# Performance work log

Measured on AMD Instinct MI355X. Metric: run time of the kernel, lower is better.

The kernel has to match this reference:

```python
import jax, jax.numpy as jnp
import numpy as np

B, T, I, H = 64, 256, 1024, 512


def _gru_layer(x, w_ih, w_hh, b_ih, b_hh):
    """PyTorch-semantics GRU layer, batch_first, h0=0.
    x: [B, T, In]; w_ih: [3H, In]; w_hh: [3H, H]; biases: [3H].
    Gate order (torch): r, z, n.
    """
    h_dim = w_hh.shape[1]
    # precompute input projections for all timesteps: [B, T, 3H]
    gx = jnp.einsum('bti,gi->btg', x, w_ih) + b_ih

    def step(h, gx_t):
        gh = h @ w_hh.T + b_hh                      # [B, 3H]
        xr, xz, xn = jnp.split(gx_t, 3, axis=-1)
        hr, hz, hn = jnp.split(gh, 3, axis=-1)
        r = jax.nn.sigmoid(xr + hr)
        z = jax.nn.sigmoid(xz + hz)
        n = jnp.tanh(xn + r * hn)
        h_new = (1.0 - z) * n + z * h
        return h_new, h_new

    h0 = jnp.zeros((x.shape[0], h_dim), x.dtype)
    _, out = jax.lax.scan(step, h0, jnp.swapaxes(gx, 0, 1))  # out: [T, B, H]
    return jnp.swapaxes(out, 0, 1)                            # [B, T, H]


def setup_inputs() -> dict:
    key = jax.random.key(0)
    ks = jax.random.split(key, 9)
    s1 = 1.0 / np.sqrt(H)   # torch GRU init: U(-1/sqrt(H), 1/sqrt(H)) of layer's hidden
    s2 = 1.0 / np.sqrt(I)
    u = lambda k, shp, s: jax.random.uniform(k, shp, jnp.float32, -s, s)
    return {
        'x': jax.random.normal(ks[0], (B, T, I), jnp.float32),
        'w_ih1': u(ks[1], (3 * H, I), s1),
        'w_hh1': u(ks[2], (3 * H, H), s1),
        'b_ih1': u(ks[3], (3 * H,), s1),
        'b_hh1': u(ks[4], (3 * H,), s1),
        'w_ih2': u(ks[5], (3 * I, H), s2),
        'w_hh2': u(ks[6], (3 * I, I), s2),
        'b_ih2': u(ks[7], (3 * I,), s2),
        'b_hh2': u(ks[8], (3 * I,), s2),
    }


def reference(x, w_ih1, w_hh1, b_ih1, b_hh1, w_ih2, w_hh2, b_ih2, b_hh2):
    h1 = _gru_layer(x, w_ih1, w_hh1, b_ih1, b_hh1)   # [B, T, H]
    h1 = jax.nn.relu(h1)
    out = _gru_layer(h1, w_ih2, w_hh2, b_ih2, b_hh2)  # [B, T, I]
    return out
```

## Files before the change

kernel.cpp:

```cpp
#include <hip/hip_runtime.h>

typedef _Float16 half_t;
typedef _Float16 half8  __attribute__((ext_vector_type(8)));
typedef float    f32x4  __attribute__((ext_vector_type(4)));
typedef int      i32x4  __attribute__((ext_vector_type(4)));

#define NB 64
#define NT 256
#define NI 1024
#define NH 512

__device__ __forceinline__ void gload16_cc(i32x4& v, const void* p) {
    asm volatile("global_load_dwordx4 %0, %1, off sc0 sc1"
                 : "=v"(v) : "v"(p) : "memory");
}
__device__ __forceinline__ void gstore16_cc(void* p, i32x4 v) {
    asm volatile("global_store_dwordx4 %0, %1, off sc0 sc1"
                 :: "v"(p), "v"(v) : "memory");
}

__device__ __forceinline__ void flag_barrier(unsigned* slots, int nslots,
                                             int my, unsigned gen, int tid) {
    if (tid < 64) {
        asm volatile("s_waitcnt vmcnt(0)" ::: "memory");
        if (tid == 0) {
            unsigned gv = gen;
            asm volatile("global_store_dword %0, %1, off sc0 sc1"
                         :: "v"(slots + my), "v"(gv) : "memory");
        }
        const unsigned* p = slots + (tid & (nslots - 1));
        int guard = 0;
        while (true) {
            unsigned v;
            asm volatile("global_load_dword %0, %1, off sc0 sc1"
                         : "=v"(v) : "v"(p) : "memory");
            asm volatile("s_waitcnt vmcnt(0)" ::: "memory");
            if (__all(v >= gen)) break;
            if (++guard > (1 << 24)) break;
        }
    }
    __syncthreads();
}

__global__ __launch_bounds__(256) void k_cvt(const float* __restrict__ s,
                                             half_t* __restrict__ d, int n4) {
    int i = blockIdx.x * 256 + threadIdx.x;
    if (i < n4) {
        float4 v = reinterpret_cast<const float4*>(s)[i];
        half_t h4[4] = {(half_t)v.x, (half_t)v.y, (half_t)v.z, (half_t)v.w};
        *reinterpret_cast<long*>(&d[i * 4]) = *reinterpret_cast<long*>(h4);
    }
}

template <int K, bool AF32>
__global__ __launch_bounds__(256) void k_gemm(const void* __restrict__ Av,
                                              const half_t* __restrict__ Bw,
                                              const float* __restrict__ bias,
                                              half_t* __restrict__ C, int N, int ldc) {
    constexpr int BK = 64;
    __shared__ half_t Al[2][128 * BK] __attribute__((aligned(16)));
    __shared__ half_t Bl[2][128 * BK] __attribute__((aligned(16)));

    const int tid = threadIdx.x, lane = tid & 63, wv = tid >> 6;
    const long m0 = (long)blockIdx.y * 128;
    const long n0 = (long)blockIdx.x * 128;
    const int wm = (wv >> 1) * 64, wn = (wv & 1) * 64;

    f32x4 acc[4][4];
#pragma unroll
    for (int nt = 0; nt < 4; ++nt) {
        float bv = bias[n0 + wn + nt * 16 + (lane & 15)];
#pragma unroll
        for (int mt = 0; mt < 4; ++mt) acc[mt][nt] = (f32x4){bv, bv, bv, bv};
    }

    auto stage = [&](int buf, int kt) {
#pragma unroll
        for (int j = 0; j < 4; ++j) {
            int c = tid + 256 * j;
            int row = c >> 3, cin = c & 7;
            int dst = row * BK + ((cin ^ (row & 7)) << 3);
            if constexpr (AF32) {
                const float* Af = (const float*)Av;
                const float* src = Af + (m0 + row) * K + kt * BK + cin * 8;
                float4 f0 = *reinterpret_cast<const float4*>(src);
                float4 f1 = *reinterpret_cast<const float4*>(src + 4);
                half8 h;
                h[0] = (half_t)f0.x; h[1] = (half_t)f0.y; h[2] = (half_t)f0.z; h[3] = (half_t)f0.w;
                h[4] = (half_t)f1.x; h[5] = (half_t)f1.y; h[6] = (half_t)f1.z; h[7] = (half_t)f1.w;
                *reinterpret_cast<half8*>(&Al[buf][dst]) = h;
            } else {
                const half_t* Ah = (const half_t*)Av;
                *reinterpret_cast<int4*>(&Al[buf][dst]) =
                    *reinterpret_cast<const int4*>(Ah + (m0 + row) * K + kt * BK + cin * 8);
            }
            *reinterpret_cast<int4*>(&Bl[buf][dst]) =
                *reinterpret_cast<const int4*>(Bw + (n0 + row) * K + kt * BK + cin * 8);
        }
    };

    stage(0, 0);
    __syncthreads();
    constexpr int NK = K / BK;
    int buf = 0;
    for (int kt = 0; kt < NK; ++kt) {
        if (kt + 1 < NK) stage(buf ^ 1, kt + 1);
        half8 af[4][2], bf[4][2];
#pragma unroll
        for (int mt = 0; mt < 4; ++mt)
#pragma unroll
            for (int ks = 0; ks < 2; ++ks) {
                int lr = wm + mt * 16 + (lane & 15);
                int off = lr * BK + ((ks * 32 + 8 * (lane >> 4)) ^ ((lr & 7) << 3));
                af[mt][ks] = *reinterpret_cast<const half8*>(&Al[buf][off]);
            }
#pragma unroll
        for (int nt = 0; nt < 4; ++nt)
#pragma unroll
            for (int ks = 0; ks < 2; ++ks) {
                int lr = wn + nt * 16 + (lane & 15);
                int off = lr * BK + ((ks * 32 + 8 * (lane >> 4)) ^ ((lr & 7) << 3));
                bf[nt][ks] = *reinterpret_cast<const half8*>(&Bl[buf][off]);
            }
#pragma unroll
        for (int mt = 0; mt < 4; ++mt)
#pragma unroll
            for (int nt = 0; nt < 4; ++nt)
#pragma unroll
                for (int ks = 0; ks < 2; ++ks)
                    acc[mt][nt] = __builtin_amdgcn_mfma_f32_16x16x32_f16(
                        af[mt][ks], bf[nt][ks], acc[mt][nt], 0, 0, 0);
        __syncthreads();
        buf ^= 1;
    }
#pragma unroll
    for (int mt = 0; mt < 4; ++mt)
#pragma unroll
        for (int nt = 0; nt < 4; ++nt)
#pragma unroll
            for (int i = 0; i < 4; ++i) {
                long row = m0 + wm + mt * 16 + 4 * (lane >> 4) + i;
                long col = n0 + wn + nt * 16 + (lane & 15);
                C[row * (long)ldc + col] = (half_t)acc[mt][nt][i];
            }
}

__global__ __launch_bounds__(256, 1) void k_phase1(const half_t* __restrict__ whh,
                                                   const float* __restrict__ bhh,
                                                   const half_t* __restrict__ gx,
                                                   half_t* __restrict__ hrelu,
                                                   half_t* __restrict__ hf16,
                                                   unsigned* __restrict__ slots) {
    __shared__ half_t wl[48 * NH] __attribute__((aligned(16)));
    __shared__ half_t hl[16 * NH] __attribute__((aligned(16)));
    __shared__ float xch[3][8][16];
    __shared__ half_t hst[8][16] __attribute__((aligned(16)));

    const int tid = threadIdx.x, lane = tid & 63, wv = tid >> 6;
    const int g = blockIdx.x & 7, memb = blockIdx.x >> 3;
    const int e0 = memb * 16;
    unsigned* gslots = slots + g * 64;

#pragma unroll
    for (int j = 0; j < 12; ++j) {
        int c = tid + 256 * j;
        int lr = c >> 6, cin = c & 63;
        int grow = (lr >> 4) * NH + e0 + (lr & 15);
        int dst = lr * NH + ((cin ^ (lr & 7)) << 3);
        *reinterpret_cast<int4*>(&wl[dst]) =
            *reinterpret_cast<const int4*>(whh + (long)grow * NH + cin * 8);
    }
#pragma unroll
    for (int j = 0; j < 2; ++j) {
        int c = tid + 256 * j;
        int lr = 8 + (c >> 6), cin = c & 63;
        int4 z; z.x = z.y = z.z = z.w = 0;
        *reinterpret_cast<int4*>(&hl[lr * NH + cin * 8]) = z;
    }
    if (tid < 16) {
        i32x4 z = (i32x4){0, 0, 0, 0};
        int bb = tid >> 1, seg = tid & 1;
        gstore16_cc(hf16 + (g * 8 + bb) * NH + e0 + seg * 8, z);
    }
    float hp = 0.f, hrp = 0.f;
    __syncthreads();
    flag_barrier(gslots, 32, memb, 1, tid);

    const float bgate = (wv < 3) ? bhh[wv * NH + e0 + (lane & 15)] : 0.f;
    const int b = tid >> 4, e = tid & 15;
    const long rb0 = (long)(g * 8 + b) * NT;

    float xr = 0.f, xz = 0.f, xn = 0.f, nxr = 0.f, nxz = 0.f, nxn = 0.f;
    if (tid < 128) {
        long gb = rb0 * 1536 + e0 + e;
        xr = (float)gx[gb]; xz = (float)gx[gb + NH]; xn = (float)gx[gb + 2 * NH];
    }

    for (int t = 0; t < NT; ++t) {
        if (tid < 128 && t > 0)
            hrelu[(rb0 + t - 1) * NH + e0 + e] = (half_t)hrp;

        const half_t* hsrc = hf16 + (t & 1) * (NB * NH);
        i32x4 sv[2];
#pragma unroll
        for (int j = 0; j < 2; ++j) {
            int c = tid + 256 * j;
            int lr = c >> 6, cin = c & 63;
            gload16_cc(sv[j], hsrc + (g * 8 + lr) * NH + cin * 8);
        }
        asm volatile("s_waitcnt vmcnt(0)" ::: "memory");
#pragma unroll
        for (int j = 0; j < 2; ++j) {
            int c = tid + 256 * j;
            int lr = c >> 6, cin = c & 63;
            *reinterpret_cast<i32x4*>(&hl[lr * NH + ((cin ^ (lr & 7)) << 3)]) = sv[j];
        }
        __syncthreads();

        if (tid < 128 && t + 1 < NT) {
            long gb = (rb0 + t + 1) * 1536 + e0 + e;
            nxr = (float)gx[gb]; nxz = (float)gx[gb + NH]; nxn = (float)gx[gb + 2 * NH];
        }

        if (wv < 3) {
            f32x4 a0 = (f32x4){bgate, bgate, bgate, bgate};
            f32x4 a1 = (f32x4){0.f, 0.f, 0.f, 0.f};
#pragma unroll
            for (int ks = 0; ks < 16; ks += 2) {
                int ar = lane & 15;
                int br = wv * 16 + (lane & 15);
                int ao0 = ar * NH + ((ks * 32 + 8 * (lane >> 4)) ^ ((ar & 7) << 3));
                int bo0 = br * NH + ((ks * 32 + 8 * (lane >> 4)) ^ ((br & 7) << 3));
                int ao1 = ar * NH + (((ks + 1) * 32 + 8 * (lane >> 4)) ^ ((ar & 7) << 3));
                int bo1 = br * NH + (((ks + 1) * 32 + 8 * (lane >> 4)) ^ ((br & 7) << 3));
                a0 = __builtin_amdgcn_mfma_f32_16x16x32_f16(
                    *reinterpret_cast<const half8*>(&hl[ao0]),
                    *reinterpret_cast<const half8*>(&wl[bo0]), a0, 0, 0, 0);
                a1 = __builtin_amdgcn_mfma_f32_16x16x32_f16(
                    *reinterpret_cast<const half8*>(&hl[ao1]),
                    *reinterpret_cast<const half8*>(&wl[bo1]), a1, 0, 0, 0);
            }
            f32x4 acc = a0 + a1;
            if (lane < 32) {
#pragma unroll
                for (int i = 0; i < 4; ++i)
                    xch[wv][4 * (lane >> 4) + i][lane & 15] = acc[i];
            }
        }
        __syncthreads();

        if (tid < 128) {
            float r = 1.f / (1.f + __expf(-(xr + xch[0][b][e])));
            float z = 1.f / (1.f + __expf(-(xz + xch[1][b][e])));
            float n = tanhf(xn + r * xch[2][b][e]);
            float hn = (1.f - z) * n + z * hp;
            hp = hn;
            hrp = fmaxf(hn, 0.f);
            hst[b][e] = (half_t)hn;
        }
        __syncthreads();

        if (t + 1 < NT) {
            if (tid < 16) {
                int bb = tid >> 1, seg = tid & 1;
                i32x4 v = *reinterpret_cast<const i32x4*>(&hst[bb][seg * 8]);
                gstore16_cc(hf16 + ((t + 1) & 1) * (NB * NH) + (g * 8 + bb) * NH + e0 + seg * 8, v);
            }
            flag_barrier(gslots, 32, memb, t + 2, tid);
        }
        xr = nxr; xz = nxz; xn = nxn;
    }
    if (tid < 128)
        hrelu[(rb0 + NT - 1) * NH + e0 + e] = (half_t)hrp;
}

__global__ __launch_bounds__(256, 1) void k_phase2(const half_t* __restrict__ whh,
                                                   const float* __restrict__ bhh,
                                                   const half_t* __restrict__ gx,
                                                   float* __restrict__ out,
                                                   half_t* __restrict__ hf16,
                                                   unsigned* __restrict__ slots) {
    __shared__ half_t wl[48 * NI] __attribute__((aligned(16)));
    __shared__ half_t hl[16 * NI] __attribute__((aligned(16)));
    __shared__ float xch2[3][16][16];
    __shared__ half_t hst[16][16] __attribute__((aligned(16)));

    const int tid = threadIdx.x, lane = tid & 63, wv = tid >> 6;
    const int xcd = blockIdx.x & 7;
    const int g = xcd >> 1;
    const int memb = ((blockIdx.x >> 3) << 1) | (xcd & 1);
    const int e0 = memb * 16;
    unsigned* gslots = slots + g * 64;

#pragma unroll
    for (int j = 0; j < 24; ++j) {
        int c = tid + 256 * j;
        int lr = c >> 7, cin = c & 127;
        int grow = (lr >> 4) * NI + e0 + (lr & 15);
        int dst = lr * NI + ((cin ^ (lr & 7)) << 3);
        *reinterpret_cast<int4*>(&wl[dst]) =
            *reinterpret_cast<const int4*>(whh + (long)grow * NI + cin * 8);
    }
    if (tid < 32) {
        i32x4 z = (i32x4){0, 0, 0, 0};
        int bb = tid >> 1, seg = tid & 1;
        gstore16_cc(hf16 + (g * 16 + bb) * NI + e0 + seg * 8, z);
    }
    float hp = 0.f;
    __syncthreads();
    flag_barrier(gslots, 64, memb, 1, tid);

    const float bgate = (wv < 3) ? bhh[wv * NI + e0 + (lane & 15)] : 0.f;
    const int b = tid >> 4, e = tid & 15;
    const long rb0 = (long)(g * 16 + b) * NT;

    float xr, xz, xn, nxr = 0.f, nxz = 0.f, nxn = 0.f;
    {
        long gb = rb0 * 3072 + e0 + e;
        xr = (float)gx[gb]; xz = (float)gx[gb + NI]; xn = (float)gx[gb + 2 * NI];
    }

    for (int t = 0; t < NT; ++t) {
        if (t > 0)
            out[(rb0 + t - 1) * NI + e0 + e] = hp;

        const half_t* hsrc = hf16 + (t & 1) * (NB * NI);
        i32x4 sv[8];
#pragma unroll
        for (int j = 0; j < 8; ++j) {
            int c = tid + 256 * j;
            int lr = c >> 7, cin = c & 127;
            gload16_cc(sv[j], hsrc + (g * 16 + lr) * NI + cin * 8);
        }
        asm volatile("s_waitcnt vmcnt(0)" ::: "memory");
#pragma unroll
        for (int j = 0; j < 8; ++j) {
            int c = tid + 256 * j;
            int lr = c >> 7, cin = c & 127;
            *reinterpret_cast<i32x4*>(&hl[lr * NI + ((cin ^ (lr & 7)) << 3)]) = sv[j];
        }
        __syncthreads();

        if (t + 1 < NT) {
            long gb = (rb0 + t + 1) * 3072 + e0 + e;
            nxr = (float)gx[gb]; nxz = (float)gx[gb + NI]; nxn = (float)gx[gb + 2 * NI];
        }

        if (wv < 3) {
            f32x4 a0 = (f32x4){bgate, bgate, bgate, bgate};
            f32x4 a1 = (f32x4){0.f, 0.f, 0.f, 0.f};
#pragma unroll
            for (int ks = 0; ks < 32; ks += 2) {
                int ar = lane & 15;
                int br = wv * 16 + (lane & 15);
                int ao0 = ar * NI + ((ks * 32 + 8 * (lane >> 4)) ^ ((ar & 7) << 3));
                int bo0 = br * NI + ((ks * 32 + 8 * (lane >> 4)) ^ ((br & 7) << 3));
                int ao1 = ar * NI + (((ks + 1) * 32 + 8 * (lane >> 4)) ^ ((ar & 7) << 3));
                int bo1 = br * NI + (((ks + 1) * 32 + 8 * (lane >> 4)) ^ ((br & 7) << 3));
                a0 = __builtin_amdgcn_mfma_f32_16x16x32_f16(
                    *reinterpret_cast<const half8*>(&hl[ao0]),
                    *reinterpret_cast<const half8*>(&wl[bo0]), a0, 0, 0, 0);
                a1 = __builtin_amdgcn_mfma_f32_16x16x32_f16(
                    *reinterpret_cast<const half8*>(&hl[ao1]),
                    *reinterpret_cast<const half8*>(&wl[bo1]), a1, 0, 0, 0);
            }
            f32x4 acc = a0 + a1;
#pragma unroll
            for (int i = 0; i < 4; ++i)
                xch2[wv][4 * (lane >> 4) + i][lane & 15] = acc[i];
        }
        __syncthreads();

        {
            float r = 1.f / (1.f + __expf(-(xr + xch2[0][b][e])));
            float z = 1.f / (1.f + __expf(-(xz + xch2[1][b][e])));
            float n = tanhf(xn + r * xch2[2][b][e]);
            float hn = (1.f - z) * n + z * hp;
            hp = hn;
            hst[b][e] = (half_t)hn;
        }
        __syncthreads();

        if (t + 1 < NT) {
            if (tid < 32) {
                int bb = tid >> 1, seg = tid & 1;
                i32x4 v = *reinterpret_cast<const i32x4*>(&hst[bb][seg * 8]);
                gstore16_cc(hf16 + ((t + 1) & 1) * (NB * NI) + (g * 16 + bb) * NI + e0 + seg * 8, v);
            }
            flag_barrier(gslots, 64, memb, t + 2, tid);
        }
        xr = nxr; xz = nxz; xn = nxn;
    }
    out[(rb0 + NT - 1) * NI + e0 + e] = hp;
}

extern "C" void kernel_launch(void* const* d_in, const int* in_sizes, int n_in,
                              void* d_out, int out_size, void* d_ws, size_t ws_size,
                              hipStream_t stream) {
    const float* x     = (const float*)d_in[0];
    const float* w_ih1 = (const float*)d_in[1];
    const float* w_hh1 = (const float*)d_in[2];
    const float* b_ih1 = (const float*)d_in[3];
    const float* b_hh1 = (const float*)d_in[4];
    const float* w_ih2 = (const float*)d_in[5];
    const float* w_hh2 = (const float*)d_in[6];
    const float* b_ih2 = (const float*)d_in[7];
    const float* b_hh2 = (const float*)d_in[8];

    char* ws = (char*)d_ws;
    unsigned* slots1 = (unsigned*)ws;
    unsigned* slots2 = (unsigned*)(ws + 2048);
    half_t* h1f16  = (half_t*)(ws + 4096);
    half_t* h2f16  = (half_t*)(ws + 135168);
    half_t* wih1h  = (half_t*)(ws + 1048576);
    half_t* whh1h  = (half_t*)(ws + 4194304);
    half_t* wih2h  = (half_t*)(ws + 5767168);
    half_t* whh2h  = (half_t*)(ws + 8912896);
    half_t* hrelu  = (half_t*)(ws + 16777216);
    half_t* gxU    = (half_t*)(ws + 50331648);
    float*  out    = (float*)d_out;

    hipMemsetAsync(ws, 0, 4096, stream);

    k_cvt<<<1536, 256, 0, stream>>>(w_ih1, wih1h, 393216);
    k_cvt<<<768,  256, 0, stream>>>(w_hh1, whh1h, 196608);
    k_cvt<<<1536, 256, 0, stream>>>(w_ih2, wih2h, 393216);
    k_cvt<<<3072, 256, 0, stream>>>(w_hh2, whh2h, 786432);

    k_gemm<1024, true><<<dim3(12, 128), 256, 0, stream>>>(x, wih1h, b_ih1, gxU, 1536, 1536);
    k_phase1<<<256, 256, 0, stream>>>(whh1h, b_hh1, gxU, hrelu, h1f16, slots1);
    k_gemm<512, false><<<dim3(24, 128), 256, 0, stream>>>(hrelu, wih2h, b_ih2, gxU, 3072, 3072);
    k_phase2<<<256, 256, 0, stream>>>(whh2h, b_hh2, gxU, out, h2f16, slots2);
}
```

Before: 2.533 ms.

## Fuse both GRU layers into one persistent kernel with wavefront pipelining

Replaces the separate layer-1 recurrence, layer-2 input GEMM and layer-2 recurrence kernels with one persistent kernel. Layer 1 runs on 64 blocks, and one wave per block computes the layer-2 input projection (with ReLU) one step behind. Layer 2 runs on 128 blocks split into two batch halves and follows layer 1 through flag waits, so the two recurrences overlap in time instead of running one after the other. It also adds s_sleep to the spin barrier. The cost is more cross-block synchronisation, a single wave carrying the extra GEMM work, and fewer blocks per recurrence group.

Result: slower. 3.281 ms (+29.5%).

```diff
diff --git a/kernel.cpp b/kernel.cpp
--- a/kernel.cpp
+++ b/kernel.cpp
@@ -9,6 +9,7 @@
 #define NT 256
 #define NI 1024
 #define NH 512
+#define MFMA16 __builtin_amdgcn_mfma_f32_16x16x32_f16
 
 __device__ __forceinline__ void gload16_cc(i32x4& v, const void* p) {
     asm volatile("global_load_dwordx4 %0, %1, off sc0 sc1"
@@ -17,6 +18,12 @@
 __device__ __forceinline__ void gstore16_cc(void* p, i32x4 v) {
     asm volatile("global_store_dwordx4 %0, %1, off sc0 sc1"
                  :: "v"(p), "v"(v) : "memory");
+}
+__device__ __forceinline__ unsigned gloadu16_cc(const void* p) {
+    unsigned v;
+    asm volatile("global_load_ushort %0, %1, off sc0 sc1"
+                 : "=v"(v) : "v"(p) : "memory");
+    return v;
 }
 
 __device__ __forceinline__ void flag_barrier(unsigned* slots, int nslots,
@@ -36,7 +43,8 @@
                          : "=v"(v) : "v"(p) : "memory");
             asm volatile("s_waitcnt vmcnt(0)" ::: "memory");
             if (__all(v >= gen)) break;
-            if (++guard > (1 << 24)) break;
+            __builtin_amdgcn_s_sleep(1);
+            if (++guard > (1 << 22)) break;
         }
     }
     __syncthreads();
@@ -52,8 +60,8 @@
     }
 }
 
-template <int K, bool AF32>
-__global__ __launch_bounds__(256) void k_gemm(const void* __restrict__ Av,
+template <int K>
+__global__ __launch_bounds__(256) void k_gemm(const float* __restrict__ Af,
                                               const half_t* __restrict__ Bw,
                                               const float* __restrict__ bias,
                                               half_t* __restrict__ C, int N, int ldc) {
@@ -80,20 +88,13 @@
             int c = tid + 256 * j;
             int row = c >> 3, cin = c & 7;
             int dst = row * BK + ((cin ^ (row & 7)) << 3);
-            if constexpr (AF32) {
-                const float* Af = (const float*)Av;
-                const float* src = Af + (m0 + row) * K + kt * BK + cin * 8;
-                float4 f0 = *reinterpret_cast<const float4*>(src);
-                float4 f1 = *reinterpret_cast<const float4*>(src + 4);
-                half8 h;
-                h[0] = (half_t)f0.x; h[1] = (half_t)f0.y; h[2] = (half_t)f0.z; h[3] = (half_t)f0.w;
-                h[4] = (half_t)f1.x; h[5] = (half_t)f1.y; h[6] = (half_t)f1.z; h[7] = (half_t)f1.w;
-                *reinterpret_cast<half8*>(&Al[buf][dst]) = h;
-            } else {
-                const half_t* Ah = (const half_t*)Av;
-                *reinterpret_cast<int4*>(&Al[buf][dst]) =
-                    *reinterpret_cast<const int4*>(Ah + (m0 + row) * K + kt * BK + cin * 8);
-            }
+            const float* src = Af + (m0 + row) * K + kt * BK + cin * 8;
+            float4 f0 = *reinterpret_cast<const float4*>(src);
+            float4 f1 = *reinterpret_cast<const float4*>(src + 4);
+            half8 h;
+            h[0] = (half_t)f0.x; h[1] = (half_t)f0.y; h[2] = (half_t)f0.z; h[3] = (half_t)f0.w;
+            h[4] = (half_t)f1.x; h[5] = (half_t)f1.y; h[6] = (half_t)f1.z; h[7] = (half_t)f1.w;
+            *reinterpret_cast<half8*>(&Al[buf][dst]) = h;
             *reinterpret_cast<int4*>(&Bl[buf][dst]) =
                 *reinterpret_cast<const int4*>(Bw + (n0 + row) * K + kt * BK + cin * 8);
         }
@@ -128,8 +129,7 @@
             for (int nt = 0; nt < 4; ++nt)
 #pragma unroll
                 for (int ks = 0; ks < 2; ++ks)
-                    acc[mt][nt] = __builtin_amdgcn_mfma_f32_16x16x32_f16(
-                        af[mt][ks], bf[nt][ks], acc[mt][nt], 0, 0, 0);
+                    acc[mt][nt] = MFMA16(af[mt][ks], bf[nt][ks], acc[mt][nt], 0, 0, 0);
         __syncthreads();
         buf ^= 1;
     }
@@ -145,253 +145,371 @@
             }
 }
 
-__global__ __launch_bounds__(256, 1) void k_phase1(const half_t* __restrict__ whh,
-                                                   const float* __restrict__ bhh,
-                                                   const half_t* __restrict__ gx,
-                                                   half_t* __restrict__ hrelu,
-                                                   half_t* __restrict__ hf16,
-                                                   unsigned* __restrict__ slots) {
-    __shared__ half_t wl[48 * NH] __attribute__((aligned(16)));
-    __shared__ half_t hl[16 * NH] __attribute__((aligned(16)));
-    __shared__ float xch[3][8][16];
-    __shared__ half_t hst[8][16] __attribute__((aligned(16)));
-
+__global__ __launch_bounds__(256, 1) void k_fused(
+    const half_t* __restrict__ whh1, const float* __restrict__ bhh1,
+    const half_t* __restrict__ wih2, const float* __restrict__ bih2,
+    const half_t* __restrict__ whh2, const float* __restrict__ bhh2,
+    half_t* gxU, float* __restrict__ out,
+    half_t* h1buf, half_t* h2buf,
+    unsigned* slots1, unsigned* slots2) {
+
+    __shared__ __attribute__((aligned(16))) char arena[160768];
     const int tid = threadIdx.x, lane = tid & 63, wv = tid >> 6;
-    const int g = blockIdx.x & 7, memb = blockIdx.x >> 3;
-    const int e0 = memb * 16;
-    unsigned* gslots = slots + g * 64;
-
-#pragma unroll
-    for (int j = 0; j < 12; ++j) {
-        int c = tid + 256 * j;
-        int lr = c >> 6, cin = c & 63;
-        int grow = (lr >> 4) * NH + e0 + (lr & 15);
-        int dst = lr * NH + ((cin ^ (lr & 7)) << 3);
-        *reinterpret_cast<int4*>(&wl[dst]) =
-            *reinterpret_cast<const int4*>(whh + (long)grow * NH + cin * 8);
+    const int bid = blockIdx.x;
+
+    if (bid < 64) {
+        half_t* wl   = (half_t*)arena;
+        half_t* wl2  = (half_t*)(arena + 32768);
+        half_t* hl   = (half_t*)(arena + 81920);
+        float*  xch  = (float* )(arena + 147456);
+        half_t* gxst = (half_t*)(arena + 153600);
+        half_t* hst  = (half_t*)(arena + 159744);
+        const int memb = bid, e0 = memb * 8;
+
+#pragma unroll
+        for (int j = 0; j < 8; ++j) {
+            int c = tid + 256 * j, lr = c >> 6, cin = c & 63;
+            i32x4 v = (i32x4){0, 0, 0, 0};
+            if (lr < 24)
+                v = *(const i32x4*)(whh1 + (long)((lr >> 3) * NH + e0 + (lr & 7)) * NH + cin * 8);
+            *(i32x4*)&wl[lr * NH + ((cin ^ (lr & 7)) << 3)] = v;
+        }
+#pragma unroll
+        for (int j = 0; j < 12; ++j) {
+            int c = tid + 256 * j, lr = c >> 6, cin = c & 63;
+            *(i32x4*)&wl2[lr * NH + ((cin ^ (lr & 7)) << 3)] =
+                *(const i32x4*)(wih2 + (long)(memb * 48 + lr) * NH + cin * 8);
+        }
+        if (tid < 64) {
+            i32x4 z = (i32x4){0, 0, 0, 0};
+            gstore16_cc(h1buf + tid * NH + e0, z);
+        }
+        __syncthreads();
+        flag_barrier(slots1, 64, memb, 1, tid);
+
+        const int e = tid & 7, b0 = tid >> 3, b1 = b0 + 32;
+        const float bh_r = bhh1[e0 + e], bh_z = bhh1[NH + e0 + e], bh_n = bhh1[2 * NH + e0 + e];
+        float bi2[3] = {0.f, 0.f, 0.f};
+        if (wv == 3) {
+#pragma unroll
+            for (int nt = 0; nt < 3; ++nt)
+                bi2[nt] = bih2[memb * 48 + nt * 16 + (lane & 15)];
+        }
+        float hp0 = 0.f, hp1 = 0.f;
+        const int cin = tid & 63, r0 = tid >> 6;
+
+        auto load_h = [&](int buf) {
+            i32x4 sv[16];
+            const half_t* hsrc = h1buf + buf * (NB * NH);
+#pragma unroll
+            for (int j = 0; j < 16; ++j)
+                gload16_cc(sv[j], hsrc + (r0 + 4 * j) * NH + cin * 8);
+            asm volatile("s_waitcnt vmcnt(0)" ::: "memory");
+            __builtin_amdgcn_sched_barrier(0);
+#pragma unroll
+            for (int j = 0; j < 16; ++j) {
+                int lr = r0 + 4 * j;
+                *(i32x4*)&hl[lr * NH + ((cin ^ (lr & 7)) << 3)] = sv[j];
+            }
+        };
+
+        auto wave3_gx2 = [&]() {
+            f32x4 g2[4][3];
+#pragma unroll
+            for (int mt = 0; mt < 4; ++mt)
+#pragma unroll
+                for (int nt = 0; nt < 3; ++nt) g2[mt][nt] = (f32x4){0.f, 0.f, 0.f, 0.f};
+#pragma unroll
+            for (int ks = 0; ks < 16; ++ks) {
+                int ko = ks * 32 + 8 * (lane >> 4);
+                half8 a[4];
+#pragma unroll
+                for (int mt = 0; mt < 4; ++mt) {
+                    int ar = mt * 16 + (lane & 15);
+                    a[mt] = *(const half8*)&hl[ar * NH + (ko ^ ((ar & 7) << 3))];
+#pragma unroll
+                    for (int jj = 0; jj < 8; ++jj)
+                        a[mt][jj] = a[mt][jj] > (half_t)0.f ? a[mt][jj] : (half_t)0.f;
+                }
+#pragma unroll
+                for (int nt = 0; nt < 3; ++nt) {
+                    int br = nt * 16 + (lane & 15);
+                    half8 bf = *(const half8*)&wl2[br * NH + (ko ^ ((br & 7) << 3))];
+#pragma unroll
+                    for (int mt = 0; mt < 4; ++mt)
+                        g2[mt][nt] = MFMA16(a[mt], bf, g2[mt][nt], 0, 0, 0);
+                }
+            }
+            int col = lane & 15, brow4 = 4 * (lane >> 4);
+#pragma unroll
+            for (int mt = 0; mt < 4; ++mt)
+#pragma unroll
+                for (int nt = 0; nt < 3; ++nt)
+#pragma unroll
+                    for (int i = 0; i < 4; ++i)
+                        gxst[(mt * 16 + brow4 + i) * 48 + nt * 16 + col] =
+                            (half_t)(g2[mt][nt][i] + bi2[nt]);
+        };
+
+        auto gx2_store = [&](int trow) {
+#pragma unroll
+            for (int rr = 0; rr < 6; ++rr) {
+                int c = tid + 64 * rr;
+                int bb = c / 6, kk = c - bb * 6;
+                gstore16_cc(gxU + ((long)bb * NT + trow) * 3072 + memb * 48 + kk * 8,
+                            *(i32x4*)&gxst[bb * 48 + kk * 8]);
+            }
+        };
+
+        for (int t = 0; t < NT; ++t) {
+            long g0 = ((long)b0 * NT + t) * 3072 + e0 + e;
+            long g1 = ((long)b1 * NT + t) * 3072 + e0 + e;
+            float xr0 = (float)gxU[g0], xz0 = (float)gxU[g0 + NH], xn0 = (float)gxU[g0 + 2 * NH];
+            float xr1 = (float)gxU[g1], xz1 = (float)gxU[g1 + NH], xn1 = (float)gxU[g1 + 2 * NH];
+            load_h(t & 1);
+            __syncthreads();
+
+            if (wv < 2) {
+#pragma unroll
+                for (int mt2 = 0; mt2 < 2; ++mt2) {
+                    const int mt = wv * 2 + mt2;
+                    f32x4 a0 = (f32x4){0, 0, 0, 0}, a1 = (f32x4){0, 0, 0, 0};
+#pragma unroll
+                    for (int ks = 0; ks < 16; ks += 2) {
+                        int ar = mt * 16 + (lane & 15);
+                        int br = lane & 15;
+                        int ko0 = ks * 32 + 8 * (lane >> 4), ko1 = ko0 + 32;
+                        a0 = MFMA16(*(const half8*)&hl[ar * NH + (ko0 ^ ((ar & 7) << 3))],
+                                    *(const half8*)&wl[br * NH + (ko0 ^ ((br & 7) << 3))], a0, 0, 0, 0);
+                        a1 = MFMA16(*(const half8*)&hl[ar * NH + (ko1 ^ ((ar & 7) << 3))],
+                                    *(const half8*)&wl[br * NH + (ko1 ^ ((br & 7) << 3))], a1, 0, 0, 0);
+                    }
+                    f32x4 acc = a0 + a1;
+                    int col = lane & 15, brow = mt * 16 + 4 * (lane >> 4);
+#pragma unroll
+                    for (int i = 0; i < 4; ++i) {
+                        if (col < 8) xch[(brow + i) * 8 + col] = acc[i];
+                        else         xch[512 + (brow + i) * 8 + (col - 8)] = acc[i];
+                    }
+                }
+            } else if (wv == 2) {
+#pragma unroll
+                for (int mt = 0; mt < 4; ++mt) {
+                    f32x4 a0 = (f32x4){0, 0, 0, 0}, a1 = (f32x4){0, 0, 0, 0};
+#pragma unroll
+                    for (int ks = 0; ks < 16; ks += 2) {
+                        int ar = mt * 16 + (lane & 15);
+                        int br = 16 + (lane & 15);
+                        int ko0 = ks * 32 + 8 * (lane >> 4), ko1 = ko0 + 32;
+                        a0 = MFMA16(*(const half8*)&hl[ar * NH + (ko0 ^ ((ar & 7) << 3))],
+                                    *(const half8*)&wl[br * NH + (ko0 ^ ((br & 7) << 3))], a0, 0, 0, 0);
+                        a1 = MFMA16(*(const half8*)&hl[ar * NH + (ko1 ^ ((ar & 7) << 3))],
+                                    *(const half8*)&wl[br * NH + (ko1 ^ ((br & 7) << 3))], a1, 0, 0, 0);
+                    }
+                    f32x4 acc = a0 + a1;
+                    int col = lane & 15, brow = mt * 16 + 4 * (lane >> 4);
+                    if (col < 8) {
+#pragma unroll
+                        for (int i = 0; i < 4; ++i)
+                            xch[1024 + (brow + i) * 8 + col] = acc[i];
+                    }
+                }
+            } else {
+                if (t > 0) wave3_gx2();
+            }
+            __syncthreads();
+
+            {
+                float dr = xch[b0 * 8 + e], dz = xch[512 + b0 * 8 + e], dn = xch[1024 + b0 * 8 + e];
+                float r = 1.f / (1.f + __expf(-(xr0 + dr + bh_r)));
+                float z = 1.f / (1.f + __expf(-(xz0 + dz + bh_z)));
+                float n = tanhf(xn0 + r * (dn + bh_n));
+                hp0 = (1.f - z) * n + z * hp0;
+                hst[b0 * 8 + e] = (half_t)hp0;
+            }
+            {
+                float dr = xch[b1 * 8 + e], dz = xch[512 + b1 * 8 + e], dn = xch[1024 + b1 * 8 + e];
+                float r = 1.f / (1.f + __expf(-(xr1 + dr + bh_r)));
+                float z = 1.f / (1.f + __expf(-(xz1 + dz + bh_z)));
+                float n = tanhf(xn1 + r * (dn + bh_n));
+                hp1 = (1.f - z) * n + z * hp1;
+                hst[b1 * 8 + e] = (half_t)hp1;
+            }
+            __syncthreads();
+
+            if (tid < 64) {
+                gstore16_cc(h1buf + ((t + 1) & 1) * (NB * NH) + tid * NH + e0,
+                            *(i32x4*)&hst[tid * 8]);
+                if (t > 0) gx2_store(t - 1);
+            }
+            flag_barrier(slots1, 64, memb, t + 2, tid);
+        }
+        load_h(NT & 1);
+        __syncthreads();
+        if (wv == 3) wave3_gx2();
+        __syncthreads();
+        if (tid < 64) {
+            gx2_store(NT - 1);
+            asm volatile("s_waitcnt vmcnt(0)" ::: "memory");
+            if (tid == 0) {
+                unsigned gv = NT + 2;
+                asm volatile("global_store_dword %0, %1, off sc0 sc1"
+                             :: "v"(slots1 + memb), "v"(gv) : "memory");
+            }
+        }
+    } else {
+        half_t* wl2h = (half_t*)arena;
+        half_t* hl2  = (half_t*)(arena + 98304);
+        float*  xch2 = (float* )(arena + 131072);
+        half_t* hst  = (half_t*)(arena + 137216);
+        const int q = (bid - 64) >> 6, memb = (bid - 64) & 63;
+        const int e0 = memb * 16;
+        unsigned* myslots = slots2 + q * 64;
+
+#pragma unroll
+        for (int j = 0; j < 24; ++j) {
+            int c = tid + 256 * j, lr = c >> 7, cin = c & 127;
+            *(i32x4*)&wl2h[lr * NI + ((cin ^ (lr & 7)) << 3)] =
+                *(const i32x4*)(whh2 + (long)((lr >> 4) * NI + e0 + (lr & 15)) * NI + cin * 8);
+        }
+        if (tid < 64) {
+            i32x4 z = (i32x4){0, 0, 0, 0};
+            gstore16_cc(h2buf + (q * 32 + (tid >> 1)) * NI + e0 + (tid & 1) * 8, z);
+        }
+        __syncthreads();
+        flag_barrier(myslots, 64, memb, 1, tid);
+        if (tid < 64) {
+            int guard = 0;
+            while (true) {
+                unsigned v;
+                asm volatile("global_load_dword %0, %1, off sc0 sc1"
+                             : "=v"(v) : "v"(slots1 + lane) : "memory");
+                asm volatile("s_waitcnt vmcnt(0)" ::: "memory");
+                if (__all(v >= 3u)) break;
+                __builtin_amdgcn_s_sleep(1);
+                if (++guard > (1 << 22)) break;
+            }
+        }
+        __syncthreads();
+
+        const int e = tid & 15, bl0 = tid >> 4, bl1 = bl0 + 16;
+        const long gb0 = (long)(q * 32 + bl0), gb1 = (long)(q * 32 + bl1);
+        const float bh_r = bhh2[e0 + e], bh_z = bhh2[NI + e0 + e], bh_n = bhh2[2 * NI + e0 + e];
+        float hp0 = 0.f, hp1 = 0.f;
+        const int cin = tid & 127, khalf = cin >> 6, cinl = cin & 63, r0 = tid >> 7;
+
+        for (int s = 0; s < NT; ++s) {
+            if (s > 0) {
+                out[(gb0 * NT + (s - 1)) * NI + e0 + e] = hp0;
+                out[(gb1 * NT + (s - 1)) * NI + e0 + e] = hp1;
+            }
+            i32x4 sv[16];
+            const half_t* hsrc = h2buf + (s & 1) * (NB * NI);
+#pragma unroll
+            for (int j = 0; j < 16; ++j)
+                gload16_cc(sv[j], hsrc + (q * 32 + r0 + 2 * j) * NI + cin * 8);
+            unsigned ur0 = gloadu16_cc(gxU + (gb0 * NT + s) * 3072 + e0 + e);
+            unsigned uz0 = gloadu16_cc(gxU + (gb0 * NT + s) * 3072 + NI + e0 + e);
+            unsigned un0 = gloadu16_cc(gxU + (gb0 * NT + s) * 3072 + 2 * NI + e0 + e);
+            unsigned ur1 = gloadu16_cc(gxU + (gb1 * NT + s) * 3072 + e0 + e);
+            unsigned uz1 = gloadu16_cc(gxU + (gb1 * NT + s) * 3072 + NI + e0 + e);
+            unsigned un1 = gloadu16_cc(gxU + (gb1 * NT + s) * 3072 + 2 * NI + e0 + e);
+            asm volatile("s_waitcnt vmcnt(0)" ::: "memory");
+            __builtin_amdgcn_sched_barrier(0);
+            float xr0 = (float)*(half_t*)&ur0, xz0 = (float)*(half_t*)&uz0, xn0 = (float)*(half_t*)&un0;
+            float xr1 = (float)*(half_t*)&ur1, xz1 = (float)*(half_t*)&uz1, xn1 = (float)*(half_t*)&un1;
+
+            f32x4 p0[2] = {(f32x4){0, 0, 0, 0}, (f32x4){0, 0, 0, 0}};
+            f32x4 p1[2] = {(f32x4){0, 0, 0, 0}, (f32x4){0, 0, 0, 0}};
+#pragma unroll
+            for (int kh = 0; kh < 2; ++kh) {
+                if (khalf == kh) {
+#pragma unroll
+                    for (int j = 0; j < 16; ++j) {
+                        int lr = r0 + 2 * j;
+                        *(i32x4*)&hl2[lr * NH + ((cinl ^ (lr & 7)) << 3)] = sv[j];
+                    }
+                }
+                __syncthreads();
+                if (wv < 3) {
+#pragma unroll
+                    for (int mt = 0; mt < 2; ++mt) {
+                        f32x4 a0 = p0[mt], a1 = p1[mt];
+#pragma unroll
+                        for (int ks = 0; ks < 16; ks += 2) {
+                            int ar = mt * 16 + (lane & 15);
+                            int br = wv * 16 + (lane & 15);
+                            int ko0 = ks * 32 + 8 * (lane >> 4), ko1 = ko0 + 32;
+                            int bk0 = kh * 512 + ko0, bk1 = kh * 512 + ko1;
+                            a0 = MFMA16(*(const half8*)&hl2[ar * NH + (ko0 ^ ((ar & 7) << 3))],
+                                        *(const half8*)&wl2h[br * NI + (bk0 ^ ((br & 7) << 3))], a0, 0, 0, 0);
+                            a1 = MFMA16(*(const half8*)&hl2[ar * NH + (ko1 ^ ((ar & 7) << 3))],
+                                        *(const half8*)&wl2h[br * NI + (bk1 ^ ((br & 7) << 3))], a1, 0, 0, 0);
+                        }
+                        p0[mt] = a0; p1[mt] = a1;
+                    }
+                }
+                __syncthreads();
+            }
+            if (wv < 3) {
+#pragma unroll
+                for (int mt = 0; mt < 2; ++mt) {
+                    f32x4 acc = p0[mt] + p1[mt];
+#pragma unroll
+                    for (int i = 0; i < 4; ++i)
+                        xch2[wv * 512 + (mt * 16 + 4 * (lane >> 4) + i) * 16 + (lane & 15)] = acc[i];
+                }
+            }
+            __syncthreads();
+
+            {
+                float dr = xch2[bl0 * 16 + e], dz = xch2[512 + bl0 * 16 + e], dn = xch2[1024 + bl0 * 16 + e];
+                float r = 1.f / (1.f + __expf(-(xr0 + dr + bh_r)));
+                float z = 1.f / (1.f + __expf(-(xz0 + dz + bh_z)));
+                float n = tanhf(xn0 + r * (dn + bh_n));
+                hp0 = (1.f - z) * n + z * hp0;
+                hst[bl0 * 16 + e] = (half_t)hp0;
+            }
+            {
+                float dr = xch2[bl1 * 16 + e], dz = xch2[512 + bl1 * 16 + e], dn = xch2[1024 + bl1 * 16 + e];
+                float r = 1.f / (1.f + __expf(-(xr1 + dr + bh_r)));
+                float z = 1.f / (1.f + __expf(-(xz1 + dz + bh_z)));
+                float n = tanhf(xn1 + r * (dn + bh_n));
+                hp1 = (1.f - z) * n + z * hp1;
+                hst[bl1 * 16 + e] = (half_t)hp1;
+            }
+            __syncthreads();
+
+            if (s + 1 < NT) {
+                if (tid < 64)
+                    gstore16_cc(h2buf + ((s + 1) & 1) * (NB * NI) + (q * 32 + (tid >> 1)) * NI + e0 + (tid & 1) * 8,
+                                *(i32x4*)&hst[(tid >> 1) * 16 + (tid & 1) * 8]);
+                if (tid < 64) {
+                    asm volatile("s_waitcnt vmcnt(0)" ::: "memory");
+                    if (tid == 0) {
+                        unsigned gv = s + 2;
+                        asm volatile("global_store_dword %0, %1, off sc0 sc1"
+                                     :: "v"(myslots + memb), "v"(gv) : "memory");
+                    }
+                    int guard = 0;
+                    while (true) {
+                        unsigned v1, v2;
+                        asm volatile("global_load_dword %0, %1, off sc0 sc1"
+                                     : "=v"(v1) : "v"(myslots + lane) : "memory");
+                        asm volatile("global_load_dword %0, %1, off sc0 sc1"
+                                     : "=v"(v2) : "v"(slots1 + lane) : "memory");
+                        asm volatile("s_waitcnt vmcnt(0)" ::: "memory");
+                        if (__all((v1 >= (unsigned)(s + 2)) && (v2 >= (unsigned)(s + 4)))) break;
+                        __builtin_amdgcn_s_sleep(1);
+                        if (++guard > (1 << 22)) break;
+                    }
+                }
+                __syncthreads();
+            }
+        }
+        out[(gb0 * NT + (NT - 1)) * NI + e0 + e] = hp0;
+        out[(gb1 * NT + (NT - 1)) * NI + e0 + e] = hp1;
     }
-#pragma unroll
-    for (int j = 0; j < 2; ++j) {
-        int c = tid + 256 * j;
-        int lr = 8 + (c >> 6), cin = c & 63;
-        int4 z; z.x = z.y = z.z = z.w = 0;
-        *reinterpret_cast<int4*>(&hl[lr * NH + cin * 8]) = z;
-    }
-    if (tid < 16) {
-        i32x4 z = (i32x4){0, 0, 0, 0};
-        int bb = tid >> 1, seg = tid & 1;
-        gstore16_cc(hf16 + (g * 8 + bb) * NH + e0 + seg * 8, z);
-    }
-    float hp = 0.f, hrp = 0.f;
-    __syncthreads();
-    flag_barrier(gslots, 32, memb, 1, tid);
-
-    const float bgate = (wv < 3) ? bhh[wv * NH + e0 + (lane & 15)] : 0.f;
-    const int b = tid >> 4, e = tid & 15;
-    const long rb0 = (long)(g * 8 + b) * NT;
-
-    float xr = 0.f, xz = 0.f, xn = 0.f, nxr = 0.f, nxz = 0.f, nxn = 0.f;
-    if (tid < 128) {
-        long gb = rb0 * 1536 + e0 + e;
-        xr = (float)gx[gb]; xz = (float)gx[gb + NH]; xn = (float)gx[gb + 2 * NH];
-    }
-
-    for (int t = 0; t < NT; ++t) {
-        if (tid < 128 && t > 0)
-            hrelu[(rb0 + t - 1) * NH + e0 + e] = (half_t)hrp;
-
-        const half_t* hsrc = hf16 + (t & 1) * (NB * NH);
-        i32x4 sv[2];
-#pragma unroll
-        for (int j = 0; j < 2; ++j) {
-            int c = tid + 256 * j;
-            int lr = c >> 6, cin = c & 63;
-            gload16_cc(sv[j], hsrc + (g * 8 + lr) * NH + cin * 8);
-        }
-        asm volatile("s_waitcnt vmcnt(0)" ::: "memory");
-#pragma unroll
-        for (int j = 0; j < 2; ++j) {
-            int c = tid + 256 * j;
-            int lr = c >> 6, cin = c & 63;
-            *reinterpret_cast<i32x4*>(&hl[lr * NH + ((cin ^ (lr & 7)) << 3)]) = sv[j];
-        }
-        __syncthreads();
-
-        if (tid < 128 && t + 1 < NT) {
-            long gb = (rb0 + t + 1) * 1536 + e0 + e;
-            nxr = (float)gx[gb]; nxz = (float)gx[gb + NH]; nxn = (float)gx[gb + 2 * NH];
-        }
-
-        if (wv < 3) {
-            f32x4 a0 = (f32x4){bgate, bgate, bgate, bgate};
-            f32x4 a1 = (f32x4){0.f, 0.f, 0.f, 0.f};
-#pragma unroll
-            for (int ks = 0; ks < 16; ks += 2) {
-                int ar = lane & 15;
-                int br = wv * 16 + (lane & 15);
-                int ao0 = ar * NH + ((ks * 32 + 8 * (lane >> 4)) ^ ((ar & 7) << 3));
-                int bo0 = br * NH + ((ks * 32 + 8 * (lane >> 4)) ^ ((br & 7) << 3));
-                int ao1 = ar * NH + (((ks + 1) * 32 + 8 * (lane >> 4)) ^ ((ar & 7) << 3));
-                int bo1 = br * NH + (((ks + 1) * 32 + 8 * (lane >> 4)) ^ ((br & 7) << 3));
-                a0 = __builtin_amdgcn_mfma_f32_16x16x32_f16(
-                    *reinterpret_cast<const half8*>(&hl[ao0]),
-                    *reinterpret_cast<const half8*>(&wl[bo0]), a0, 0, 0, 0);
-                a1 = __builtin_amdgcn_mfma_f32_16x16x32_f16(
-                    *reinterpret_cast<const half8*>(&hl[ao1]),
-                    *reinterpret_cast<const half8*>(&wl[bo1]), a1, 0, 0, 0);
-            }
-            f32x4 acc = a0 + a1;
-            if (lane < 32) {
-#pragma unroll
-                for (int i = 0; i < 4; ++i)
-                    xch[wv][4 * (lane >> 4) + i][lane & 15] = acc[i];
-            }
-        }
-        __syncthreads();
-
-        if (tid < 128) {
-            float r = 1.f / (1.f + __expf(-(xr + xch[0][b][e])));
-            float z = 1.f / (1.f + __expf(-(xz + xch[1][b][e])));
-            float n = tanhf(xn + r * xch[2][b][e]);
-            float hn = (1.f - z) * n + z * hp;
-            hp = hn;
-            hrp = fmaxf(hn, 0.f);
-            hst[b][e] = (half_t)hn;
-        }
-        __syncthreads();
-
-        if (t + 1 < NT) {
-            if (tid < 16) {
-                int bb = tid >> 1, seg = tid & 1;
-                i32x4 v = *reinterpret_cast<const i32x4*>(&hst[bb][seg * 8]);
-                gstore16_cc(hf16 + ((t + 1) & 1) * (NB * NH) + (g * 8 + bb) * NH + e0 + seg * 8, v);
-            }
-            flag_barrier(gslots, 32, memb, t + 2, tid);
-        }
-        xr = nxr; xz = nxz; xn = nxn;
-    }
-    if (tid < 128)
-        hrelu[(rb0 + NT - 1) * NH + e0 + e] = (half_t)hrp;
-}
-
-__global__ __launch_bounds__(256, 1) void k_phase2(const half_t* __restrict__ whh,
-                                                   const float* __restrict__ bhh,
-                                                   const half_t* __restrict__ gx,
-                                                   float* __restrict__ out,
-                                                   half_t* __restrict__ hf16,
-                                                   unsigned* __restrict__ slots) {
-    __shared__ half_t wl[48 * NI] __attribute__((aligned(16)));
-    __shared__ half_t hl[16 * NI] __attribute__((aligned(16)));
-    __shared__ float xch2[3][16][16];
-    __shared__ half_t hst[16][16] __attribute__((aligned(16)));
-
-    const int tid = threadIdx.x, lane = tid & 63, wv = tid >> 6;
-    const int xcd = blockIdx.x & 7;
-    const int g = xcd >> 1;
-    const int memb = ((blockIdx.x >> 3) << 1) | (xcd & 1);
-    const int e0 = memb * 16;
-    unsigned* gslots = slots + g * 64;
-
-#pragma unroll
-    for (int j = 0; j < 24; ++j) {
-        int c = tid + 256 * j;
-        int lr = c >> 7, cin = c & 127;
-        int grow = (lr >> 4) * NI + e0 + (lr & 15);
-        int dst = lr * NI + ((cin ^ (lr & 7)) << 3);
-        *reinterpret_cast<int4*>(&wl[dst]) =
-            *reinterpret_cast<const int4*>(whh + (long)grow * NI + cin * 8);
-    }
-    if (tid < 32) {
-        i32x4 z = (i32x4){0, 0, 0, 0};
-        int bb = tid >> 1, seg = tid & 1;
-        gstore16_cc(hf16 + (g * 16 + bb) * NI + e0 + seg * 8, z);
-    }
-    float hp = 0.f;
-    __syncthreads();
-    flag_barrier(gslots, 64, memb, 1, tid);
-
-    const float bgate = (wv < 3) ? bhh[wv * NI + e0 + (lane & 15)] : 0.f;
-    const int b = tid >> 4, e = tid & 15;
-    const long rb0 = (long)(g * 16 + b) * NT;
-
-    float xr, xz, xn, nxr = 0.f, nxz = 0.f, nxn = 0.f;
-    {
-        long gb = rb0 * 3072 + e0 + e;
-        xr = (float)gx[gb]; xz = (float)gx[gb + NI]; xn = (float)gx[gb + 2 * NI];
-    }
-
-    for (int t = 0; t < NT; ++t) {
-        if (t > 0)
-            out[(rb0 + t - 1) * NI + e0 + e] = hp;
-
-        const half_t* hsrc = hf16 + (t & 1) * (NB * NI);
-        i32x4 sv[8];
-#pragma unroll
-        for (int j = 0; j < 8; ++j) {
-            int c = tid + 256 * j;
-            int lr = c >> 7, cin = c & 127;
-            gload16_cc(sv[j], hsrc + (g * 16 + lr) * NI + cin * 8);
-        }
-        asm volatile("s_waitcnt vmcnt(0)" ::: "memory");
-#pragma unroll
-        for (int j = 0; j < 8; ++j) {
-            int c = tid + 256 * j;
-            int lr = c >> 7, cin = c & 127;
-            *reinterpret_cast<i32x4*>(&hl[lr * NI + ((cin ^ (lr & 7)) << 3)]) = sv[j];
-        }
-        __syncthreads();
-
-        if (t + 1 < NT) {
-            long gb = (rb0 + t + 1) * 3072 + e0 + e;
-            nxr = (float)gx[gb]; nxz = (float)gx[gb + NI]; nxn = (float)gx[gb + 2 * NI];
-        }
-
-        if (wv < 3) {
-            f32x4 a0 = (f32x4){bgate, bgate, bgate, bgate};
-            f32x4 a1 = (f32x4){0.f, 0.f, 0.f, 0.f};
-#pragma unroll
-            for (int ks = 0; ks < 32; ks += 2) {
-                int ar = lane & 15;
-                int br = wv * 16 + (lane & 15);
-                int ao0 = ar * NI + ((ks * 32 + 8 * (lane >> 4)) ^ ((ar & 7) << 3));
-                int bo0 = br * NI + ((ks * 32 + 8 * (lane >> 4)) ^ ((br & 7) << 3));
-                int ao1 = ar * NI + (((ks + 1) * 32 + 8 * (lane >> 4)) ^ ((ar & 7) << 3));
-                int bo1 = br * NI + (((ks + 1) * 32 + 8 * (lane >> 4)) ^ ((br & 7) << 3));
-                a0 = __builtin_amdgcn_mfma_f32_16x16x32_f16(
-                    *reinterpret_cast<const half8*>(&hl[ao0]),
-                    *reinterpret_cast<const half8*>(&wl[bo0]), a0, 0, 0, 0);
-                a1 = __builtin_amdgcn_mfma_f32_16x16x32_f16(
-                    *reinterpret_cast<const half8*>(&hl[ao1]),
-                    *reinterpret_cast<const half8*>(&wl[bo1]), a1, 0, 0, 0);
-            }
-            f32x4 acc = a0 + a1;
-#pragma unroll
-            for (int i = 0; i < 4; ++i)
-                xch2[wv][4 * (lane >> 4) + i][lane & 15] = acc[i];
-        }
-        __syncthreads();
-
-        {
-            float r = 1.f / (1.f + __expf(-(xr + xch2[0][b][e])));
-            float z = 1.f / (1.f + __expf(-(xz + xch2[1][b][e])));
-            float n = tanhf(xn + r * xch2[2][b][e]);
-            float hn = (1.f - z) * n + z * hp;
-            hp = hn;
-            hst[b][e] = (half_t)hn;
-        }
-        __syncthreads();
-
-        if (t + 1 < NT) {
-            if (tid < 32) {
-                int bb = tid >> 1, seg = tid & 1;
-                i32x4 v = *reinterpret_cast<const i32x4*>(&hst[bb][seg * 8]);
-                gstore16_cc(hf16 + ((t + 1) & 1) * (NB * NI) + (g * 16 + bb) * NI + e0 + seg * 8, v);
-            }
-            flag_barrier(gslots, 64, memb, t + 2, tid);
-        }
-        xr = nxr; xz = nxz; xn = nxn;
-    }
-    out[(rb0 + NT - 1) * NI + e0 + e] = hp;
 }
 
 extern "C" void kernel_launch(void* const* d_in, const int* in_sizes, int n_in,
@@ -409,15 +527,14 @@
 
     char* ws = (char*)d_ws;
     unsigned* slots1 = (unsigned*)ws;
-    unsigned* slots2 = (unsigned*)(ws + 2048);
-    half_t* h1f16  = (half_t*)(ws + 4096);
-    half_t* h2f16  = (half_t*)(ws + 135168);
+    unsigned* slots2 = (unsigned*)(ws + 1024);
+    half_t* h1buf  = (half_t*)(ws + 4096);
+    half_t* h2buf  = (half_t*)(ws + 135168);
     half_t* wih1h  = (half_t*)(ws + 1048576);
     half_t* whh1h  = (half_t*)(ws + 4194304);
     half_t* wih2h  = (half_t*)(ws + 5767168);
     half_t* whh2h  = (half_t*)(ws + 8912896);
-    half_t* hrelu  = (half_t*)(ws + 16777216);
-    half_t* gxU    = (half_t*)(ws + 50331648);
+    half_t* gxU    = (half_t*)(ws + 16777216);
     float*  out    = (float*)d_out;
 
     hipMemsetAsync(ws, 0, 4096, stream);
@@ -427,8 +544,7 @@
     k_cvt<<<1536, 256, 0, stream>>>(w_ih2, wih2h, 393216);
     k_cvt<<<3072, 256, 0, stream>>>(w_hh2, whh2h, 786432);
 
-    k_gemm<1024, true><<<dim3(12, 128), 256, 0, stream>>>(x, wih1h, b_ih1, gxU, 1536, 1536);
-    k_phase1<<<256, 256, 0, stream>>>(whh1h, b_hh1, gxU, hrelu, h1f16, slots1);
-    k_gemm<512, false><<<dim3(24, 128), 256, 0, stream>>>(hrelu, wih2h, b_ih2, gxU, 3072, 3072);
-    k_phase2<<<256, 256, 0, stream>>>(whh2h, b_hh2, gxU, out, h2f16, slots2);
-}
+    k_gemm<1024><<<dim3(12, 128), 256, 0, stream>>>(x, wih1h, b_ih1, gxU, 1536, 3072);
+    k_fused<<<192, 256, 0, stream>>>(whh1h, b_hh1, wih2h, b_ih2, whh2h, b_hh2,
+                                     gxU, out, h1buf, h2buf, slots1, slots2);
+}
```
